# Optimization experiments

Hardware: AMD Instinct MI355X
Metric: run time of the kernel (lower is better)

The kernel has to match this reference:

```python
import jax, jax.numpy as jnp
import numpy as np
import math

B, S, H = 8, 1024, 1024
NUM_LABELS = 2

# torch nn.Linear weight [out,in]; we store transposed [in,out] so y = x @ W + b

def _mha(x, mask, qw, qb, kw, kb, vw, vb, ow, ob, n_heads):
    b, s, h = x.shape
    d = h // n_heads
    Q = (x @ qw + qb).reshape(b, s, n_heads, d)
    K = (x @ kw + kb).reshape(b, s, n_heads, d)
    V = (x @ vw + vb).reshape(b, s, n_heads, d)
    scores = jnp.einsum('bqhd,bkhd->bhqk', Q, K) / math.sqrt(d)  # [b,h,s,s]
    if mask is not None:
        scores = jnp.where(mask[:, None, None, :] == 0, jnp.asarray(-1e9, scores.dtype), scores)
    w = jax.nn.softmax(scores, axis=-1)  # dropout is identity in eval mode
    ctx = jnp.einsum('bhqk,bkhd->bqhd', w, V).reshape(b, s, h)
    return ctx @ ow + ob, w


def _linear_params(key, fin, fout):
    k1, k2 = jax.random.split(key)
    lim = 1.0 / math.sqrt(fin)
    w = jax.random.uniform(k1, (fin, fout), jnp.float32, -lim, lim)
    b = jax.random.uniform(k2, (fout,), jnp.float32, -lim, lim)
    return w, b


def setup_inputs() -> dict:
    key = jax.random.key(0)
    ks = jax.random.split(key, 20)
    inp = {
        'hidden_states': jax.random.normal(ks[0], (B, S, H), jnp.float32),
        'attention_mask': jax.random.randint(ks[1], (B, S), 0, 2, jnp.int32),
    }
    i = 2
    for pre in ('beh', 'tmp', 'pat'):
        for nm in ('q', 'k', 'v', 'o'):
            w, b = _linear_params(ks[i], H, H)
            inp[f'{pre}_{nm}w'] = w
            inp[f'{pre}_{nm}b'] = b
            i += 1
    inp['fus1_w'], inp['fus1_b'] = _linear_params(ks[i], 3 * H, H); i += 1
    inp['fus2_w'], inp['fus2_b'] = _linear_params(ks[i], H, H // 2); i += 1
    inp['cls_w'], inp['cls_b'] = _linear_params(ks[i], H // 2, NUM_LABELS)
    return inp


def reference(hidden_states, attention_mask,
              beh_qw, beh_qb, beh_kw, beh_kb, beh_vw, beh_vb, beh_ow, beh_ob,
              tmp_qw, tmp_qb, tmp_kw, tmp_kb, tmp_vw, tmp_vb, tmp_ow, tmp_ob,
              pat_qw, pat_qb, pat_kw, pat_kb, pat_vw, pat_vb, pat_ow, pat_ob,
              fus1_w, fus1_b, fus2_w, fus2_b, cls_w, cls_b):
    beh_out, _ = _mha(hidden_states, attention_mask, beh_qw, beh_qb, beh_kw, beh_kb, beh_vw, beh_vb, beh_ow, beh_ob, 8)
    tmp_out, _ = _mha(hidden_states, attention_mask, tmp_qw, tmp_qb, tmp_kw, tmp_kb, tmp_vw, tmp_vb, tmp_ow, tmp_ob, 4)
    pat_out, _ = _mha(hidden_states, attention_mask, pat_qw, pat_qb, pat_kw, pat_kb, pat_vw, pat_vb, pat_ow, pat_ob, 4)
    m = attention_mask[:, :, None].astype(hidden_states.dtype)  # [B,S,1]
    denom = m.sum(axis=1)  # [B,1] broadcast like torch expand_as sum
    beh_p = (beh_out * m).sum(axis=1) / denom
    tmp_p = (tmp_out * m).sum(axis=1) / denom
    pat_p = (pat_out * m).sum(axis=1) / denom
    fused = jnp.concatenate([beh_p, tmp_p, pat_p], axis=-1)  # [B,3H]
    h1 = jax.nn.relu(fused @ fus1_w + fus1_b)
    h2 = jax.nn.relu(h1 @ fus2_w + fus2_b)
    logits = h2 @ cls_w + cls_b
    return logits
```

## Files before the change

### kernel.cpp

```cpp
#include <hip/hip_runtime.h>

#define DEVINL __device__ __forceinline__
typedef __attribute__((ext_vector_type(8))) __bf16 bf16x8;
typedef __attribute__((ext_vector_type(4))) __bf16 bf16x4;
typedef __attribute__((ext_vector_type(4))) float f32x4;

DEVINL void gload16(void* lds, const void* g) {
  __builtin_amdgcn_global_load_lds((const __attribute__((address_space(1))) void*)g,
                                   (__attribute__((address_space(3))) void*)lds, 16, 0, 0);
}

__global__ void cvt_bf16_kernel(const float* __restrict__ in, __bf16* __restrict__ out, int n4) {
  int i = blockIdx.x * 256 + threadIdx.x;
  if (i >= n4) return;
  float4 v = reinterpret_cast<const float4*>(in)[i];
  bf16x4 o;
  o.x = (__bf16)v.x; o.y = (__bf16)v.y; o.z = (__bf16)v.z; o.w = (__bf16)v.w;
  reinterpret_cast<bf16x4*>(out)[i] = o;
}

__global__ void wt_pack_kernel(const float* __restrict__ Wq, const float* __restrict__ Wk,
                               const float* __restrict__ Wv, __bf16* __restrict__ WT) {
  __shared__ float t[64][65];
  int k0 = blockIdx.x * 64;
  int n0 = blockIdx.y * 64;
  const float* W = (n0 < 1024) ? Wq : (n0 < 2048 ? Wk : Wv);
  int nn0 = n0 & 1023;
  int r = threadIdx.x >> 6, c = threadIdx.x & 63;
#pragma unroll
  for (int i = 0; i < 16; ++i)
    t[r + i*4][c] = W[(size_t)(k0 + r + i*4) * 1024 + nn0 + c];
  __syncthreads();
#pragma unroll
  for (int i = 0; i < 16; ++i) {
    int row = r + i*4;
    WT[(size_t)(n0 + row) * 1024 + k0 + c] = (__bf16)t[c][row];
  }
}

__global__ __launch_bounds__(256) void gemm_qkv_kernel(
    const __bf16* __restrict__ A, const __bf16* __restrict__ WT,
    const float* __restrict__ bq, const float* __restrict__ bk, const float* __restrict__ bv,
    __bf16* __restrict__ C) {
  constexpr int N_ = 3072, K_ = 1024;
  __shared__ __align__(16) __bf16 As[128*64];
  __shared__ __align__(16) __bf16 Bs[128*64];
  int tid = threadIdx.x;
  int lane = tid & 63, wave = tid >> 6;
  int l15 = lane & 15, l4 = lane >> 4;
  int wr = wave >> 1, wc = wave & 1;
  int flat = blockIdx.y * 24 + blockIdx.x;
  int swz  = (flat & 7) * 192 + (flat >> 3);
  int m0 = (swz & 63) * 128;
  int n0 = (swz >> 6) * 128;

  f32x4 acc[4][4] = {};

  for (int kt = 0; kt < K_/64; ++kt) {
#pragma unroll
    for (int it = 0; it < 4; ++it) {
      int c = it*256 + tid;
      int row = c >> 3, cc = c & 7;
      const char* gA = (const char*)(A  + (size_t)(m0+row)*K_ + kt*64) + cc*16;
      const char* gB = (const char*)(WT + (size_t)(n0+row)*K_ + kt*64) + cc*16;
      char* lA = (char*)As + (it*256 + (tid & ~63))*16;
      char* lB = (char*)Bs + (it*256 + (tid & ~63))*16;
      gload16(lA, gA);
      gload16(lB, gB);
    }
    __syncthreads();
#pragma unroll
    for (int ks = 0; ks < 2; ++ks) {
      bf16x8 af[4], bfr[4];
#pragma unroll
      for (int m = 0; m < 4; ++m)
        af[m] = *(const bf16x8*)(As + (wr*64 + m*16 + l15)*64 + ks*32 + l4*8);
#pragma unroll
      for (int n = 0; n < 4; ++n)
        bfr[n] = *(const bf16x8*)(Bs + (wc*64 + n*16 + l15)*64 + ks*32 + l4*8);
#pragma unroll
      for (int m = 0; m < 4; ++m)
#pragma unroll
        for (int n = 0; n < 4; ++n)
          acc[m][n] = __builtin_amdgcn_mfma_f32_16x16x32_bf16(af[m], bfr[n], acc[m][n], 0, 0, 0);
    }
    __syncthreads();
  }
#pragma unroll
  for (int n = 0; n < 4; ++n) {
    int col = n0 + wc*64 + n*16 + l15;
    const float* bias = (col < 1024) ? bq : (col < 2048 ? bk : bv);
    float bv_ = bias[col & 1023];
#pragma unroll
    for (int m = 0; m < 4; ++m) {
      int rowb = m0 + wr*64 + m*16 + l4*4;
#pragma unroll
      for (int r = 0; r < 4; ++r)
        C[(size_t)(rowb + r)*N_ + col] = (__bf16)(acc[m][n][r] + bv_);
    }
  }
}

__global__ void vt_pack_kernel(const __bf16* __restrict__ QKV, __bf16* __restrict__ Vt,
                               int hcnt, int D) {
  __shared__ __bf16 t[64][65];
  int s0 = blockIdx.x * 64, d0 = blockIdx.y * 64;
  int bh = blockIdx.z;
  int b = bh / hcnt, h = bh - b*hcnt;
  int r = threadIdx.x >> 6, c = threadIdx.x & 63;
  const __bf16* src = QKV + (size_t)b*1024*3072 + 2048 + (size_t)h*D;
#pragma unroll
  for (int i = 0; i < 16; ++i)
    t[r + i*4][c] = src[(size_t)(s0 + r + i*4)*3072 + d0 + c];
  __syncthreads();
  __bf16* dst = Vt + ((size_t)bh*D + d0)*1024 + s0;
#pragma unroll
  for (int i = 0; i < 16; ++i) {
    int row = r + i*4;
    dst[(size_t)row*1024 + c] = t[c][row];
  }
}

template<int D, int WQ, int HCNT>
__global__ __launch_bounds__(256) void attn_kernel(
    const __bf16* __restrict__ QKV, const __bf16* __restrict__ Vt,
    const int* __restrict__ mask, float* __restrict__ ctx) {
  constexpr int QT  = 4*WQ;
  constexpr int MT  = WQ/16;
  constexpr int KC  = D/32;
  constexpr int NT2 = D/16;
  constexpr int CPR = D/8;
  __shared__ __align__(16) __bf16 smem[64*D + D*64 + 4*WQ*72];
  __shared__ float Ml[64];
  __bf16* Kl = smem;
  __bf16* Vl = smem + 64*D;
  __bf16* Pl = smem + 128*D;

  int tid = threadIdx.x;
  int lane = tid & 63, wave = tid >> 6;
  int l15 = lane & 15, l4 = lane >> 4;
  int q0 = blockIdx.x * QT;
  int h = blockIdx.y, b = blockIdx.z;
  int bh = b*HCNT + h;
  const float scale = (D == 128) ? 0.08838834764831845f : 0.0625f;

  {
    const char* qbase = (const char*)(QKV + (size_t)(b*1024 + q0)*3072 + (size_t)h*D);
    for (int c0 = 0; c0 < QT*D/8; c0 += 256) {
      int c = c0 + tid;
      int row = c / CPR, cc = c % CPR;
      gload16((char*)smem + (c0 + (tid & ~63))*16,
              qbase + (size_t)row*6144 + ((cc ^ (row & 7))*16));
    }
  }
  __syncthreads();
  bf16x8 qf[MT][KC];
#pragma unroll
  for (int m = 0; m < MT; ++m)
#pragma unroll
    for (int kc = 0; kc < KC; ++kc) {
      int row = wave*WQ + m*16 + l15;
      int boff = ((kc*32 + l4*8)*2) ^ ((row & 7) << 4);
      qf[m][kc] = *(const bf16x8*)((const char*)smem + (size_t)row*(D*2) + boff);
    }
  __syncthreads();

  f32x4 ao[MT][NT2] = {};
  float dsum[MT][4] = {};

  const char* kbase = (const char*)(QKV + (size_t)(b*1024)*3072 + 1024 + (size_t)h*D);
  const char* vbase = (const char*)(Vt + (size_t)bh*D*1024);

  for (int t = 0; t < 16; ++t) {
    for (int c0 = 0; c0 < 8*D; c0 += 256) {
      int c = c0 + tid;
      int row = c / CPR, cc = c % CPR;
      gload16((char*)Kl + (c0 + (tid & ~63))*16,
              kbase + (size_t)(t*64 + row)*6144 + ((cc ^ (row & 7))*16));
    }
    for (int c0 = 0; c0 < 8*D; c0 += 256) {
      int c = c0 + tid;
      int row = c >> 3, cc = c & 7;
      gload16((char*)Vl + (c0 + (tid & ~63))*16,
              vbase + (size_t)row*2048 + t*128 + ((cc ^ (row & 7))*16));
    }
    if (tid < 64) Ml[tid] = (float)mask[b*1024 + t*64 + tid];
    __syncthreads();

#pragma unroll
    for (int n = 0; n < 4; ++n) {
      f32x4 s[MT] = {};
#pragma unroll
      for (int kc = 0; kc < KC; ++kc) {
        int krow = n*16 + l15;
        int boff = ((kc*32 + l4*8)*2) ^ ((krow & 7) << 4);
        bf16x8 kf = *(const bf16x8*)((const char*)Kl + (size_t)krow*(D*2) + boff);
#pragma unroll
        for (int m = 0; m < MT; ++m)
          s[m] = __builtin_amdgcn_mfma_f32_16x16x32_bf16(qf[m][kc], kf, s[m], 0, 0, 0);
      }
      float mv = Ml[n*16 + l15];
#pragma unroll
      for (int m = 0; m < MT; ++m)
#pragma unroll
        for (int r = 0; r < 4; ++r) {
          float pf_ = __expf(s[m][r] * scale) * mv;
          __bf16 pb = (__bf16)pf_;
          dsum[m][r] += (float)pb;
          Pl[(size_t)(wave*WQ + m*16 + l4*4 + r)*72 + n*16 + l15] = pb;
        }
    }
    bf16x8 pfr[MT][2];
#pragma unroll
    for (int m = 0; m < MT; ++m)
#pragma unroll
      for (int kk = 0; kk < 2; ++kk)
        pfr[m][kk] = *(const bf16x8*)(Pl + (size_t)(wave*WQ + m*16 + l15)*72 + kk*32 + l4*8);
#pragma unroll
    for (int n2 = 0; n2 < NT2; ++n2) {
      bf16x8 vf[2];
#pragma unroll
      for (int kk = 0; kk < 2; ++kk) {
        int vrow = n2*16 + l15;
        int boff = ((kk*32 + l4*8)*2) ^ ((vrow & 7) << 4);
        vf[kk] = *(const bf16x8*)((const char*)Vl + (size_t)vrow*128 + boff);
      }
#pragma unroll
      for (int m = 0; m < MT; ++m)
#pragma unroll
        for (int kk = 0; kk < 2; ++kk)
          ao[m][n2] = __builtin_amdgcn_mfma_f32_16x16x32_bf16(pfr[m][kk], vf[kk], ao[m][n2], 0, 0, 0);
    }
    __syncthreads();
  }

  float inv[MT][4];
#pragma unroll
  for (int m = 0; m < MT; ++m)
#pragma unroll
    for (int r = 0; r < 4; ++r) {
      float v = dsum[m][r];
      v += __shfl_xor(v, 1, 64);
      v += __shfl_xor(v, 2, 64);
      v += __shfl_xor(v, 4, 64);
      v += __shfl_xor(v, 8, 64);
      inv[m][r] = 1.0f / v;
    }
#pragma unroll
  for (int m = 0; m < MT; ++m) {
    int rowb = b*1024 + q0 + wave*WQ + m*16 + l4*4;
#pragma unroll
    for (int n2 = 0; n2 < NT2; ++n2) {
      int col = h*D + n2*16 + l15;
#pragma unroll
      for (int r = 0; r < 4; ++r)
        ctx[(size_t)(rowb + r)*1024 + col] = ao[m][n2][r] * inv[m][r];
    }
  }
}

__global__ void denom_kernel(const int* __restrict__ mask, float* __restrict__ denom) {
  int b = blockIdx.x, t = threadIdx.x;
  int acc = 0;
  for (int s = t; s < 1024; s += 256) acc += mask[b*1024 + s];
  for (int o = 32; o; o >>= 1) acc += __shfl_down(acc, o, 64);
  __shared__ int red[4];
  if ((t & 63) == 0) red[t >> 6] = acc;
  __syncthreads();
  if (t == 0) denom[b] = (float)(red[0] + red[1] + red[2] + red[3]);
}

__global__ void pool_partial_kernel(const float* __restrict__ ctx, const int* __restrict__ mask,
                                    float* __restrict__ part) {
  int sc = blockIdx.x;
  int b  = blockIdx.y;
  int t  = threadIdx.x;
  const float* base = ctx + (size_t)b*1024*1024 + (size_t)sc*32*1024;
  const int* mrow = mask + b*1024 + sc*32;
  float4 acc = {0.f, 0.f, 0.f, 0.f};
  for (int s = 0; s < 32; ++s) {
    if (mrow[s]) {
      float4 v = reinterpret_cast<const float4*>(base + (size_t)s*1024)[t];
      acc.x += v.x; acc.y += v.y; acc.z += v.z; acc.w += v.w;
    }
  }
  reinterpret_cast<float4*>(part + ((size_t)b*32 + sc)*1024)[t] = acc;
}

__global__ void pool_reduce_kernel(const float* __restrict__ part, const float* __restrict__ denom,
                                   float* __restrict__ out) {
  int i = blockIdx.x*256 + threadIdx.x;
  int b = i >> 10, c = i & 1023;
  float a = 0.f;
#pragma unroll
  for (int sc = 0; sc < 32; ++sc) a += part[((size_t)b*32 + sc)*1024 + c];
  out[i] = a / denom[b];
}

__global__ void oproj_partial_kernel(const float* __restrict__ pooled,
    const float* __restrict__ W0, const float* __restrict__ W1, const float* __restrict__ W2,
    float* __restrict__ part) {
  int ai = blockIdx.z;
  const float* W = (ai == 0) ? W0 : (ai == 1 ? W1 : W2);
  int ks = blockIdx.y, k0 = ks*128;
  __shared__ float xl[8*128];
  const float* P = pooled + ai*8192;
  for (int i = threadIdx.x; i < 8*128; i += 256) {
    int b = i >> 7, kk = i & 127;
    xl[i] = P[b*1024 + k0 + kk];
  }
  __syncthreads();
  int n = blockIdx.x*256 + threadIdx.x;
  float acc[8] = {};
  for (int kk = 0; kk < 128; ++kk) {
    float w = W[(size_t)(k0+kk)*1024 + n];
#pragma unroll
    for (int b = 0; b < 8; ++b) acc[b] += xl[b*128 + kk] * w;
  }
#pragma unroll
  for (int b = 0; b < 8; ++b) part[(((size_t)ai*8 + ks)*8 + b)*1024 + n] = acc[b];
}

__global__ void oproj_reduce_kernel(const float* __restrict__ part,
    const float* __restrict__ b0, const float* __restrict__ b1, const float* __restrict__ b2,
    float* __restrict__ fused) {
  int i = blockIdx.x*256 + threadIdx.x;
  int ai = i >> 13, rem = i & 8191;
  int b = rem >> 10, n = rem & 1023;
  const float* bb = (ai == 0) ? b0 : (ai == 1 ? b1 : b2);
  float a = bb[n];
#pragma unroll
  for (int ks = 0; ks < 8; ++ks) a += part[(((size_t)ai*8 + ks)*8 + b)*1024 + n];
  fused[b*3072 + ai*1024 + n] = a;
}

__global__ void fc_partial_kernel(const float* __restrict__ X, const float* __restrict__ W,
                                  float* __restrict__ part, int Kin, int Nout, int kchunk) {
  extern __shared__ float xl[];
  int ks = blockIdx.y, k0 = ks*kchunk;
  for (int i = threadIdx.x; i < 8*kchunk; i += 256) {
    int b = i / kchunk, kk = i - b*kchunk;
    xl[i] = X[b*Kin + k0 + kk];
  }
  __syncthreads();
  int n = blockIdx.x*256 + threadIdx.x;
  float acc[8] = {};
  for (int kk = 0; kk < kchunk; ++kk) {
    float w = W[(size_t)(k0+kk)*Nout + n];
#pragma unroll
    for (int b = 0; b < 8; ++b) acc[b] += xl[b*kchunk + kk] * w;
  }
#pragma unroll
  for (int b = 0; b < 8; ++b) part[((size_t)ks*8 + b)*Nout + n] = acc[b];
}

__global__ void fc_reduce_kernel(const float* __restrict__ part, const float* __restrict__ bias,
                                 float* __restrict__ out, int Nout, int KS, int do_relu) {
  int i = blockIdx.x*256 + threadIdx.x;
  int b = i / Nout, n = i - b*Nout;
  float a = bias[n];
  for (int ks = 0; ks < KS; ++ks) a += part[((size_t)ks*8 + b)*Nout + n];
  out[i] = do_relu ? fmaxf(a, 0.f) : a;
}

__global__ void cls_kernel(const float* __restrict__ h2, const float* __restrict__ W,
                           const float* __restrict__ bias, float* __restrict__ out) {
  int t = threadIdx.x;
  int o = t >> 4, sl = t & 15;
  int b = o >> 1, n = o & 1;
  float a = 0.f;
  for (int k = sl; k < 512; k += 16) a += h2[b*512 + k] * W[k*2 + n];
#pragma unroll
  for (int m = 1; m < 16; m <<= 1) a += __shfl_xor(a, m, 64);
  if (sl == 0) out[o] = a + bias[n];
}

extern "C" void kernel_launch(void* const* d_in, const int* in_sizes, int n_in,
                              void* d_out, int out_size, void* d_ws, size_t ws_size,
                              hipStream_t stream) {
  const float* X   = (const float*)d_in[0];
  const int* mask  = (const int*)d_in[1];
  const float* w_[3][8];
  for (int a = 0; a < 3; ++a)
    for (int j = 0; j < 8; ++j)
      w_[a][j] = (const float*)d_in[2 + a*8 + j];
  const float* fus1_w = (const float*)d_in[26];
  const float* fus1_b = (const float*)d_in[27];
  const float* fus2_w = (const float*)d_in[28];
  const float* fus2_b = (const float*)d_in[29];
  const float* cls_w  = (const float*)d_in[30];
  const float* cls_b  = (const float*)d_in[31];

  char* p = (char*)d_ws;
  auto carve = [&](size_t bytes) { char* r = p; p += (bytes + 255) & ~(size_t)255; return r; };
  __bf16* Xb    = (__bf16*)carve((size_t)8192*1024*2);
  __bf16* WTb   = (__bf16*)carve((size_t)3072*1024*2);
  __bf16* QKVb  = (__bf16*)carve((size_t)8192*3072*2);
  __bf16* Vtb   = (__bf16*)carve((size_t)8192*1024*2);
  float* ctxb   = (float*)carve((size_t)8192*1024*4);
  float* pooledb= (float*)carve(3*8*1024*4);
  float* denomb = (float*)carve(256);
  float* fusedb = (float*)carve(8*3072*4);
  float* partb  = (float*)carve((size_t)24*8*1024*4);
  float* opartb = (float*)carve((size_t)3*8*8*1024*4);
  float* poolpartb = (float*)carve((size_t)8*32*1024*4);
  float* h1b    = (float*)carve(8*1024*4);
  float* h2b    = (float*)carve(8*512*4);
  if ((size_t)(p - (char*)d_ws) > ws_size) return;

  cvt_bf16_kernel<<<8192, 256, 0, stream>>>(X, Xb, 8192*1024/4);
  denom_kernel<<<8, 256, 0, stream>>>(mask, denomb);

  for (int a = 0; a < 3; ++a) {
    wt_pack_kernel<<<dim3(16,48), 256, 0, stream>>>(w_[a][0], w_[a][2], w_[a][4], WTb);
    gemm_qkv_kernel<<<dim3(24,64), 256, 0, stream>>>(Xb, WTb, w_[a][1], w_[a][3], w_[a][5], QKVb);
    if (a == 0) {
      vt_pack_kernel<<<dim3(16,2,64), 256, 0, stream>>>(QKVb, Vtb, 8, 128);
      attn_kernel<128,32,8><<<dim3(8,8,8), 256, 0, stream>>>(QKVb, Vtb, mask, ctxb);
    } else {
      vt_pack_kernel<<<dim3(16,4,32), 256, 0, stream>>>(QKVb, Vtb, 4, 256);
      attn_kernel<256,16,4><<<dim3(16,4,8), 256, 0, stream>>>(QKVb, Vtb, mask, ctxb);
    }
    pool_partial_kernel<<<dim3(32,8), 256, 0, stream>>>(ctxb, mask, poolpartb);
    pool_reduce_kernel<<<32, 256, 0, stream>>>(poolpartb, denomb, pooledb + a*8192);
  }

  oproj_partial_kernel<<<dim3(4,8,3), 256, 0, stream>>>(pooledb,
      w_[0][6], w_[1][6], w_[2][6], opartb);
  oproj_reduce_kernel<<<96, 256, 0, stream>>>(opartb,
      w_[0][7], w_[1][7], w_[2][7], fusedb);
  fc_partial_kernel<<<dim3(4,24), 256, 8*128*4, stream>>>(fusedb, fus1_w, partb, 3072, 1024, 128);
  fc_reduce_kernel<<<32, 256, 0, stream>>>(partb, fus1_b, h1b, 1024, 24, 1);
  fc_partial_kernel<<<dim3(2,8), 256, 8*128*4, stream>>>(h1b, fus2_w, partb, 1024, 512, 128);
  fc_reduce_kernel<<<16, 256, 0, stream>>>(partb, fus2_b, h2b, 512, 8, 1);
  cls_kernel<<<1, 256, 0, stream>>>(h2b, cls_w, cls_b, (float*)d_out);
}
```

Before: 548.5 us.

## Double-buffer QKV GEMM with swizzled LDS and larger 128x256 tiles

Rewrites the QKV projection GEMM to use a 128x256 output tile with 512 threads (8 waves). It double-buffers LDS so the global-to-LDS loads for the next K step overlap the MFMA work on the current one, and XOR-swizzles the LDS layout to avoid bank conflicts. MFMA sections get raised wave priority. The trade-off is higher LDS use (about 96KB), which cuts occupancy, and the tile-order swizzle for L2 locality is dropped.

```diff
diff --git a/kernel.cpp b/kernel.cpp
--- a/kernel.cpp
+++ b/kernel.cpp
@@ -38,65 +38,92 @@
   }
 }
 
-__global__ __launch_bounds__(256) void gemm_qkv_kernel(
+__global__ __launch_bounds__(512) void gemm_qkv_kernel(
     const __bf16* __restrict__ A, const __bf16* __restrict__ WT,
     const float* __restrict__ bq, const float* __restrict__ bk, const float* __restrict__ bv,
     __bf16* __restrict__ C) {
   constexpr int N_ = 3072, K_ = 1024;
-  __shared__ __align__(16) __bf16 As[128*64];
-  __shared__ __align__(16) __bf16 Bs[128*64];
+  __shared__ __align__(16) __bf16 lds[2][(128 + 256) * 64];
   int tid = threadIdx.x;
-  int lane = tid & 63, wave = tid >> 6;
+  int lane = tid & 63;
+  int wave = tid >> 6;
   int l15 = lane & 15, l4 = lane >> 4;
-  int wr = wave >> 1, wc = wave & 1;
-  int flat = blockIdx.y * 24 + blockIdx.x;
-  int swz  = (flat & 7) * 192 + (flat >> 3);
-  int m0 = (swz & 63) * 128;
-  int n0 = (swz >> 6) * 128;
+  int wr = wave >> 2, wc = wave & 3;
+  int n0 = blockIdx.x * 256, m0 = blockIdx.y * 128;
 
   f32x4 acc[4][4] = {};
 
-  for (int kt = 0; kt < K_/64; ++kt) {
-#pragma unroll
-    for (int it = 0; it < 4; ++it) {
-      int c = it*256 + tid;
-      int row = c >> 3, cc = c & 7;
-      const char* gA = (const char*)(A  + (size_t)(m0+row)*K_ + kt*64) + cc*16;
-      const char* gB = (const char*)(WT + (size_t)(n0+row)*K_ + kt*64) + cc*16;
-      char* lA = (char*)As + (it*256 + (tid & ~63))*16;
-      char* lB = (char*)Bs + (it*256 + (tid & ~63))*16;
-      gload16(lA, gA);
-      gload16(lB, gB);
-    }
-    __syncthreads();
-#pragma unroll
-    for (int ks = 0; ks < 2; ++ks) {
+  const char* Abase = (const char*)(A  + (size_t)m0 * K_);
+  const char* Bbase = (const char*)(WT + (size_t)n0 * K_);
+
+  auto STAGE = [&](int buf, int kt) {
+    char* Al = (char*)lds[buf];
+    char* Bl = (char*)(lds[buf] + 128 * 64);
+#pragma unroll
+    for (int i = 0; i < 2; ++i) {
+      int c = i * 512 + tid;
+      int r = c >> 3, cc = c & 7, g = cc ^ (r & 7);
+      gload16(Al + (size_t)(c & ~63) * 16,
+              Abase + (size_t)r * (K_ * 2) + kt * 128 + g * 16);
+    }
+#pragma unroll
+    for (int i = 0; i < 4; ++i) {
+      int c = i * 512 + tid;
+      int r = c >> 3, cc = c & 7, g = cc ^ (r & 7);
+      gload16(Bl + (size_t)(c & ~63) * 16,
+              Bbase + (size_t)r * (K_ * 2) + kt * 128 + g * 16);
+    }
+  };
+
+  int cur = 0;
+  STAGE(0, 0);
+  for (int kt = 0; kt < 16; ++kt) {
+    if (kt < 15) {
+      STAGE(cur ^ 1, kt + 1);
+      asm volatile("s_waitcnt vmcnt(6)" ::: "memory");
+    } else {
+      asm volatile("s_waitcnt vmcnt(0)" ::: "memory");
+    }
+    __builtin_amdgcn_s_barrier();
+    const char* Al = (const char*)lds[cur];
+    const char* Bl = (const char*)(lds[cur] + 128 * 64);
+#pragma unroll
+    for (int kk = 0; kk < 2; ++kk) {
       bf16x8 af[4], bfr[4];
-#pragma unroll
-      for (int m = 0; m < 4; ++m)
-        af[m] = *(const bf16x8*)(As + (wr*64 + m*16 + l15)*64 + ks*32 + l4*8);
-#pragma unroll
-      for (int n = 0; n < 4; ++n)
-        bfr[n] = *(const bf16x8*)(Bs + (wc*64 + n*16 + l15)*64 + ks*32 + l4*8);
+      int j = kk * 4 + l4;
+#pragma unroll
+      for (int m = 0; m < 4; ++m) {
+        int row = wr * 64 + m * 16 + l15;
+        af[m] = *(const bf16x8*)(Al + ((size_t)row * 8 + (j ^ (row & 7))) * 16);
+      }
+#pragma unroll
+      for (int n = 0; n < 4; ++n) {
+        int row = wc * 64 + n * 16 + l15;
+        bfr[n] = *(const bf16x8*)(Bl + ((size_t)row * 8 + (j ^ (row & 7))) * 16);
+      }
+      __builtin_amdgcn_s_setprio(1);
 #pragma unroll
       for (int m = 0; m < 4; ++m)
 #pragma unroll
         for (int n = 0; n < 4; ++n)
           acc[m][n] = __builtin_amdgcn_mfma_f32_16x16x32_bf16(af[m], bfr[n], acc[m][n], 0, 0, 0);
-    }
-    __syncthreads();
-  }
+      __builtin_amdgcn_s_setprio(0);
+    }
+    __builtin_amdgcn_s_barrier();
+    cur ^= 1;
+  }
+
 #pragma unroll
   for (int n = 0; n < 4; ++n) {
-    int col = n0 + wc*64 + n*16 + l15;
+    int col = n0 + wc * 64 + n * 16 + l15;
     const float* bias = (col < 1024) ? bq : (col < 2048 ? bk : bv);
     float bv_ = bias[col & 1023];
 #pragma unroll
     for (int m = 0; m < 4; ++m) {
-      int rowb = m0 + wr*64 + m*16 + l4*4;
+      int rowb = m0 + wr * 64 + m * 16 + l4 * 4;
 #pragma unroll
       for (int r = 0; r < 4; ++r)
-        C[(size_t)(rowb + r)*N_ + col] = (__bf16)(acc[m][n][r] + bv_);
+        C[(size_t)(rowb + r) * N_ + col] = (__bf16)(acc[m][n][r] + bv_);
     }
   }
 }
@@ -413,7 +440,7 @@
 
   for (int a = 0; a < 3; ++a) {
     wt_pack_kernel<<<dim3(16,48), 256, 0, stream>>>(w_[a][0], w_[a][2], w_[a][4], WTb);
-    gemm_qkv_kernel<<<dim3(24,64), 256, 0, stream>>>(Xb, WTb, w_[a][1], w_[a][3], w_[a][5], QKVb);
+    gemm_qkv_kernel<<<dim3(12,64), 512, 0, stream>>>(Xb, WTb, w_[a][1], w_[a][3], w_[a][5], QKVb);
     if (a == 0) {
       vt_pack_kernel<<<dim3(16,2,64), 256, 0, stream>>>(QKVb, Vtb, 8, 128);
       attn_kernel<128,32,8><<<dim3(8,8,8), 256, 0, stream>>>(QKVb, Vtb, mask, ctxb);
```

Measured after the change: 507.3 us. 7.5% less time.
